# Kernel tuning notes

Hardware: AMD Instinct MI355X
Metric: run time of the kernel (lower is better)

The kernel has to match this reference:

```python
import jax, jax.numpy as jnp
import numpy as np

B, T, C, H = 16, 2048, 768, 128

def setup_inputs() -> dict:
    key = jax.random.key(0)
    k1, k2, k3, k4 = jax.random.split(key, 4)
    x = jax.random.normal(k1, (B, T, C), dtype=jnp.float32)
    Wq = jax.random.normal(k2, (C, H), dtype=jnp.float32) * (C ** -0.5)
    Wk = jax.random.normal(k3, (C, H), dtype=jnp.float32) * (C ** -0.5)
    Wv = jax.random.normal(k4, (C, H), dtype=jnp.float32) * (C ** -0.5)
    return {"x": x, "Wq": Wq, "Wk": Wk, "Wv": Wv}

def reference(x, Wq, Wk, Wv):
    Bc, Tc, Cc = x.shape
    q = jnp.einsum('btc,ch->bth', x, Wq)
    k = jnp.einsum('btc,ch->bth', x, Wk)
    v = jnp.einsum('btc,ch->bth', x, Wv)
    wei = jnp.einsum('bqh,bkh->bqk', q, k)  # [B,T,T]
    tril = jnp.tril(jnp.ones((Tc, Tc), dtype=jnp.float32))
    # Faithful to original: mask with -inf FIRST, then scale by C**-0.5
    wei = jnp.where(tril == 0, -jnp.inf, wei) * (Cc ** -0.5)
    wei = jax.nn.softmax(wei, axis=-1)
    out = jnp.einsum('bqk,bkh->bqh', wei, v)
    return out
```

## Files before the change

### kernel.cpp

```cpp
#include <hip/hip_runtime.h>
#include <hip/hip_bf16.h>
#include <cstdint>

#define B_ 16
#define T_ 2048
#define C_ 768
#define H_ 128

typedef __bf16 bf16x8 __attribute__((ext_vector_type(8)));
typedef float f32x4 __attribute__((ext_vector_type(4)));
typedef unsigned short u16x8 __attribute__((ext_vector_type(8)));

__device__ __forceinline__ void gld_lds16(const void* g, void* s) {
    __builtin_amdgcn_global_load_lds(
        (__attribute__((address_space(1))) void*)(size_t)g,
        (__attribute__((address_space(3))) void*)s,
        16, 0, 0);
}

__device__ __forceinline__ unsigned short f2bf(float f) {
    __bf16 h = (__bf16)f;
    return __builtin_bit_cast(unsigned short, h);
}

__global__ __launch_bounds__(256) void wxconv_kernel(
    const float* __restrict__ Wq, const float* __restrict__ Wk,
    const float* __restrict__ Wv, const float* __restrict__ x,
    unsigned short* __restrict__ wT, unsigned short* __restrict__ xb) {
    int bidx = blockIdx.x;
    if (bidx < 1152) {
        int idx = bidx * 256 + threadIdx.x;
        if (idx >= 3 * H_ * C_) return;
        int w = idx / (H_ * C_);
        int r = idx % (H_ * C_);
        int h = r / C_;
        int c = r % C_;
        const float* W = (w == 0) ? Wq : ((w == 1) ? Wk : Wv);
        wT[idx] = f2bf(W[c * H_ + h]);
    } else {
        size_t i = ((size_t)(bidx - 1152) * 256 + threadIdx.x) * 8;
        f32x4 a = *(const f32x4*)(x + i);
        f32x4 b = *(const f32x4*)(x + i + 4);
        u16x8 o;
        o[0] = f2bf(a[0]); o[1] = f2bf(a[1]); o[2] = f2bf(a[2]); o[3] = f2bf(a[3]);
        o[4] = f2bf(b[0]); o[5] = f2bf(b[1]); o[6] = f2bf(b[2]); o[7] = f2bf(b[3]);
        *(u16x8*)(xb + i) = o;
    }
}

__global__ __launch_bounds__(256, 2) void proj_kernel(
    const unsigned short* __restrict__ xb, const unsigned short* __restrict__ wT,
    unsigned short* __restrict__ qb, unsigned short* __restrict__ kb,
    unsigned short* __restrict__ vtb) {
    __shared__ unsigned short Asm[64 * 64];
    __shared__ unsigned short Bsm[384 * 64];

    const int tid = threadIdx.x;
    const int m0 = blockIdx.x * 64;
    const int wid = tid >> 6;
    const int lane = tid & 63;
    const int quad = lane >> 4;
    const int lo16 = lane & 15;
    const int wn = wid * 96;

    f32x4 acc[4][6] = {};

    for (int kt = 0; kt < 12; ++kt) {
        const int k0 = kt * 64;
        __syncthreads();
#pragma unroll
        for (int rnd = 0; rnd < 2; ++rnd) {
            int cidx = rnd * 256 + tid;
            int m = cidx >> 3;
            int c = (cidx & 7) ^ (m & 7);
            gld_lds16((const char*)xb + ((size_t)(m0 + m) * C_ + k0 + c * 8) * 2,
                      (char*)Asm + (rnd * 256 + wid * 64) * 16);
        }
#pragma unroll
        for (int rnd = 0; rnd < 12; ++rnd) {
            int cidx = rnd * 256 + tid;
            int n = cidx >> 3;
            int c = (cidx & 7) ^ (n & 7);
            gld_lds16((const char*)wT + ((size_t)(n >> 7) * (H_ * C_) + (n & 127) * C_ + k0 + c * 8) * 2,
                      (char*)Bsm + (rnd * 256 + wid * 64) * 16);
        }
        __syncthreads();

#pragma unroll
        for (int kk = 0; kk < 2; ++kk) {
            bf16x8 afrag[4], bfrag[6];
#pragma unroll
            for (int mi = 0; mi < 4; ++mi) {
                int m = mi * 16 + lo16;
                int c = (kk * 4 + quad) ^ (m & 7);
                afrag[mi] = *(const bf16x8*)((const __bf16*)Asm + m * 64 + c * 8);
            }
#pragma unroll
            for (int ni = 0; ni < 6; ++ni) {
                int n = wn + ni * 16 + lo16;
                int c = (kk * 4 + quad) ^ (n & 7);
                bfrag[ni] = *(const bf16x8*)((const __bf16*)Bsm + n * 64 + c * 8);
            }
#pragma unroll
            for (int mi = 0; mi < 4; ++mi)
#pragma unroll
                for (int ni = 0; ni < 6; ++ni)
                    acc[mi][ni] = __builtin_amdgcn_mfma_f32_16x16x32_bf16(
                        afrag[mi], bfrag[ni], acc[mi][ni], 0, 0, 0);
        }
    }

#pragma unroll
    for (int mi = 0; mi < 4; ++mi) {
        int grow = m0 + mi * 16 + quad * 4;
#pragma unroll
        for (int ni = 0; ni < 6; ++ni) {
            int n = wn + ni * 16 + lo16;
            int wmat = n >> 7;
            int col = n & 127;
            if (wmat < 2) {
                unsigned short* o = (wmat == 0) ? qb : kb;
#pragma unroll
                for (int rr = 0; rr < 4; ++rr)
                    o[(size_t)(grow + rr) * H_ + col] = f2bf(acc[mi][ni][rr]);
            } else {
                int b = grow >> 11;
                int t = grow & 2047;
                ushort4 pk;
                pk.x = f2bf(acc[mi][ni][0]); pk.y = f2bf(acc[mi][ni][1]);
                pk.z = f2bf(acc[mi][ni][2]); pk.w = f2bf(acc[mi][ni][3]);
                *(ushort4*)(vtb + ((size_t)b * H_ + col) * T_ + t) = pk;
            }
        }
    }
}

__device__ __forceinline__ void attn_seg(
    const unsigned short* kB, const unsigned short* vB, const bf16x8 qfrag[4],
    int j0, int j1, int jmask, float& l_part, f32x4 oacc[8],
    unsigned short* Ks, unsigned short* Vs, unsigned short* Pw,
    int tid, int wid, int quad, int lo16) {
    const float cs = 0.05205877694341f;
    for (int j = j0; j < j1; ++j) {
        const int kv0 = j * 64;
        __syncthreads();
#pragma unroll
        for (int rnd = 0; rnd < 4; ++rnd) {
            int cidx = rnd * 256 + tid;
            int m = cidx >> 4;
            int c = (cidx & 15) ^ (m & 15);
            gld_lds16((const char*)kB + ((size_t)(kv0 + m) * H_ + c * 8) * 2,
                      (char*)Ks + (rnd * 256 + wid * 64) * 16);
        }
#pragma unroll
        for (int rnd = 0; rnd < 4; ++rnd) {
            int cidx = rnd * 256 + tid;
            int d = cidx >> 3;
            int c = (cidx & 7) ^ (d & 7);
            gld_lds16((const char*)vB + ((size_t)d * T_ + kv0 + c * 8) * 2,
                      (char*)Vs + (rnd * 256 + wid * 64) * 16);
        }
        __syncthreads();

        f32x4 s[4] = {};
#pragma unroll
        for (int ks = 0; ks < 4; ++ks) {
#pragma unroll
            for (int ni = 0; ni < 4; ++ni) {
                int row = ni * 16 + lo16;
                int slot = (ks * 4 + quad) ^ lo16;
                bf16x8 kf = *(const bf16x8*)((const __bf16*)Ks + row * 128 + slot * 8);
                s[ni] = __builtin_amdgcn_mfma_f32_16x16x32_bf16(kf, qfrag[ks], s[ni], 0, 0, 0);
            }
        }

        const bool diag = (j == jmask);
        if (diag) {
#pragma unroll
            for (int ni = 0; ni < 4; ++ni) {
#pragma unroll
                for (int rr = 0; rr < 4; ++rr) {
                    float p = exp2f(s[ni][rr] * cs);
                    if (ni * 16 + quad * 4 + rr > wid * 16 + lo16) p = 0.f;
                    l_part += p;
                    s[ni][rr] = p;
                }
                ushort4 w4;
                w4.x = f2bf(s[ni][0]); w4.y = f2bf(s[ni][1]);
                w4.z = f2bf(s[ni][2]); w4.w = f2bf(s[ni][3]);
                *(ushort4*)(Pw + lo16 * 72 + ni * 16 + quad * 4) = w4;
            }
        } else {
#pragma unroll
            for (int ni = 0; ni < 4; ++ni) {
#pragma unroll
                for (int rr = 0; rr < 4; ++rr) {
                    float p = exp2f(s[ni][rr] * cs);
                    l_part += p;
                    s[ni][rr] = p;
                }
                ushort4 w4;
                w4.x = f2bf(s[ni][0]); w4.y = f2bf(s[ni][1]);
                w4.z = f2bf(s[ni][2]); w4.w = f2bf(s[ni][3]);
                *(ushort4*)(Pw + lo16 * 72 + ni * 16 + quad * 4) = w4;
            }
        }

#pragma unroll
        for (int ks2 = 0; ks2 < 2; ++ks2) {
            bf16x8 pf = *(const bf16x8*)((const __bf16*)Pw + lo16 * 72 + ks2 * 32 + quad * 8);
#pragma unroll
            for (int nd = 0; nd < 8; ++nd) {
                int dn = nd * 16 + lo16;
                int vc = (ks2 * 4 + quad) ^ (dn & 7);
                bf16x8 vf = *(const bf16x8*)((const __bf16*)Vs + dn * 64 + vc * 8);
                oacc[nd] = __builtin_amdgcn_mfma_f32_16x16x32_bf16(pf, vf, oacc[nd], 0, 0, 0);
            }
        }
    }
}

__device__ __forceinline__ void load_qfrag(const unsigned short* qB, int q0,
                                           int wid, int quad, int lo16, bf16x8 qf[4]) {
    const unsigned short* qrow = qB + (size_t)(q0 + wid * 16 + lo16) * H_ + quad * 8;
#pragma unroll
    for (int ks = 0; ks < 4; ++ks) qf[ks] = *(const bf16x8*)(qrow + ks * 32);
}

__global__ __launch_bounds__(256, 2) void attn_kernel(
    const unsigned short* __restrict__ qb, const unsigned short* __restrict__ kb,
    const unsigned short* __restrict__ vtb, float* __restrict__ out,
    float* __restrict__ pO, float* __restrict__ pL) {
    __shared__ unsigned short Ks[64 * 128];
    __shared__ unsigned short Vs[128 * 64];
    __shared__ unsigned short Ps[4][16 * 72];

    const int tid = threadIdx.x;
    const int bid = blockIdx.x;
    const int half = bid >> 8;
    const int slot = bid & 255;
    const int r = slot >> 4;
    const int b = slot & 15;

    const unsigned short* qB = qb + (size_t)b * T_ * H_;
    const unsigned short* kB = kb + (size_t)b * T_ * H_;
    const unsigned short* vB = vtb + (size_t)b * H_ * T_;

    const int wid = tid >> 6;
    const int lane = tid & 63;
    const int quad = lane >> 4;
    const int lo16 = lane & 15;
    unsigned short* Pw = &Ps[wid][0];

    const int qtb = 31 - r;
    bf16x8 qf[4];
    float l_part = 0.f;
    f32x4 oacc[8] = {};

    if (half == 0) {
        load_qfrag(qB, r * 64, wid, quad, lo16, qf);
        attn_seg(kB, vB, qf, 0, r + 1, r, l_part, oacc, Ks, Vs, Pw, tid, wid, quad, lo16);
        l_part += __shfl_xor(l_part, 16);
        l_part += __shfl_xor(l_part, 32);
#pragma unroll
        for (int rr = 0; rr < 4; ++rr) {
            float lv = __shfl(l_part, quad * 4 + rr);
            float inv = 1.0f / lv;
            int qrow = r * 64 + wid * 16 + quad * 4 + rr;
            float* orow = out + ((size_t)b * T_ + qrow) * H_;
#pragma unroll
            for (int nd = 0; nd < 8; ++nd)
                orow[nd * 16 + lo16] = oacc[nd][rr] * inv;
        }
        l_part = 0.f;
#pragma unroll
        for (int nd = 0; nd < 8; ++nd) oacc[nd] = f32x4{0.f, 0.f, 0.f, 0.f};
        load_qfrag(qB, qtb * 64, wid, quad, lo16, qf);
        attn_seg(kB, vB, qf, 0, 16 - r, -1, l_part, oacc, Ks, Vs, Pw, tid, wid, quad, lo16);
    } else {
        load_qfrag(qB, qtb * 64, wid, quad, lo16, qf);
        attn_seg(kB, vB, qf, 16 - r, 32 - r, qtb, l_part, oacc, Ks, Vs, Pw, tid, wid, quad, lo16);
    }

    l_part += __shfl_xor(l_part, 16);
    l_part += __shfl_xor(l_part, 32);
    float* myO = pO + (size_t)(half * 256 + slot) * (64 * 128);
    if (lane < 16) pL[(half * 256 + slot) * 64 + wid * 16 + lo16] = l_part;
#pragma unroll
    for (int rr = 0; rr < 4; ++rr) {
        int ql = wid * 16 + quad * 4 + rr;
#pragma unroll
        for (int nd = 0; nd < 8; ++nd)
            myO[ql * 128 + nd * 16 + lo16] = oacc[nd][rr];
    }
}

__global__ __launch_bounds__(256) void combine_kernel(
    const float* __restrict__ pO, const float* __restrict__ pL,
    float* __restrict__ out) {
    const int slot = blockIdx.x;
    const int r = slot >> 4;
    const int b = slot & 15;
    const int q0 = (31 - r) * 64;
    __shared__ float ls[64];
    const int tid = threadIdx.x;
    if (tid < 64) ls[tid] = pL[slot * 64 + tid] + pL[(256 + slot) * 64 + tid];
    __syncthreads();
    const float* O0 = pO + (size_t)slot * (64 * 128);
    const float* O1 = pO + (size_t)(256 + slot) * (64 * 128);
    float* ob = out + ((size_t)b * T_ + q0) * H_;
#pragma unroll
    for (int k = 0; k < 8; ++k) {
        int idx = (k * 256 + tid) * 4;
        f32x4 a = *(const f32x4*)(O0 + idx);
        f32x4 c = *(const f32x4*)(O1 + idx);
        float inv = 1.0f / ls[idx >> 7];
        f32x4 o;
        o[0] = (a[0] + c[0]) * inv; o[1] = (a[1] + c[1]) * inv;
        o[2] = (a[2] + c[2]) * inv; o[3] = (a[3] + c[3]) * inv;
        *(f32x4*)(ob + idx) = o;
    }
}

extern "C" void kernel_launch(void* const* d_in, const int* in_sizes, int n_in,
                              void* d_out, int out_size, void* d_ws, size_t ws_size,
                              hipStream_t stream) {
    const float* x = (const float*)d_in[0];
    const float* Wq = (const float*)d_in[1];
    const float* Wk = (const float*)d_in[2];
    const float* Wv = (const float*)d_in[3];
    float* out = (float*)d_out;

    char* ws = (char*)d_ws;
    unsigned short* wT  = (unsigned short*)ws;
    unsigned short* qb  = (unsigned short*)(ws + (1ull << 20));
    unsigned short* kb  = (unsigned short*)(ws + (9ull << 20));
    unsigned short* vtb = (unsigned short*)(ws + (17ull << 20));
    unsigned short* xb  = (unsigned short*)(ws + (25ull << 20));
    float* pO = (float*)(ws + (80ull << 20));
    float* pL = (float*)(ws + (100ull << 20));

    hipLaunchKernelGGL(wxconv_kernel, dim3(13440), dim3(256), 0, stream, Wq, Wk, Wv, x, wT, xb);
    hipLaunchKernelGGL(proj_kernel, dim3(512), dim3(256), 0, stream, xb, wT, qb, kb, vtb);
    hipLaunchKernelGGL(attn_kernel, dim3(512), dim3(256), 0, stream, qb, kb, vtb, out, pO, pL);
    hipLaunchKernelGGL(combine_kernel, dim3(256), dim3(256), 0, stream, pO, pL, out);
}
```

Baseline: 221.6 us.

## Fuse x bf16 conversion into projection and double-buffer projection and attention tiles

The separate x-to-bf16 conversion pass is removed. The projection kernel now reads fp32 x directly, converts it in registers and writes it into LDS. Projection is retiled into 512-thread blocks of 128 rows by 192 columns, with double-buffered LDS so the next k-slice loads while MFMAs run. Attention also double-buffers its K/V tiles, issuing the next tile's async loads before computing on the current one, which drops one barrier per iteration. This costs more LDS, which may reduce occupancy, and adds register pressure from the fp32 prefetch.

```diff
diff --git a/kernel.cpp b/kernel.cpp
--- a/kernel.cpp
+++ b/kernel.cpp
@@ -23,99 +23,136 @@
     return __builtin_bit_cast(unsigned short, h);
 }
 
-__global__ __launch_bounds__(256) void wxconv_kernel(
+__global__ __launch_bounds__(256) void wconv_kernel(
     const float* __restrict__ Wq, const float* __restrict__ Wk,
-    const float* __restrict__ Wv, const float* __restrict__ x,
-    unsigned short* __restrict__ wT, unsigned short* __restrict__ xb) {
-    int bidx = blockIdx.x;
-    if (bidx < 1152) {
-        int idx = bidx * 256 + threadIdx.x;
-        if (idx >= 3 * H_ * C_) return;
-        int w = idx / (H_ * C_);
-        int r = idx % (H_ * C_);
-        int h = r / C_;
-        int c = r % C_;
-        const float* W = (w == 0) ? Wq : ((w == 1) ? Wk : Wv);
-        wT[idx] = f2bf(W[c * H_ + h]);
-    } else {
-        size_t i = ((size_t)(bidx - 1152) * 256 + threadIdx.x) * 8;
-        f32x4 a = *(const f32x4*)(x + i);
-        f32x4 b = *(const f32x4*)(x + i + 4);
-        u16x8 o;
-        o[0] = f2bf(a[0]); o[1] = f2bf(a[1]); o[2] = f2bf(a[2]); o[3] = f2bf(a[3]);
-        o[4] = f2bf(b[0]); o[5] = f2bf(b[1]); o[6] = f2bf(b[2]); o[7] = f2bf(b[3]);
-        *(u16x8*)(xb + i) = o;
-    }
-}
-
-__global__ __launch_bounds__(256, 2) void proj_kernel(
-    const unsigned short* __restrict__ xb, const unsigned short* __restrict__ wT,
+    const float* __restrict__ Wv, unsigned short* __restrict__ wT) {
+    int idx = blockIdx.x * 256 + threadIdx.x;
+    if (idx >= 3 * H_ * C_) return;
+    int w = idx / (H_ * C_);
+    int r = idx % (H_ * C_);
+    int h = r / C_;
+    int c = r % C_;
+    const float* W = (w == 0) ? Wq : ((w == 1) ? Wk : Wv);
+    wT[idx] = f2bf(W[c * H_ + h]);
+}
+
+__global__ __launch_bounds__(512, 2) void proj_kernel(
+    const float* __restrict__ x, const unsigned short* __restrict__ wT,
     unsigned short* __restrict__ qb, unsigned short* __restrict__ kb,
     unsigned short* __restrict__ vtb) {
-    __shared__ unsigned short Asm[64 * 64];
-    __shared__ unsigned short Bsm[384 * 64];
+    __shared__ unsigned short Asm[2][128 * 64];
+    __shared__ unsigned short Bsm[2][192 * 64];
 
     const int tid = threadIdx.x;
-    const int m0 = blockIdx.x * 64;
+    const int nh = blockIdx.x & 1;
+    const int m0 = (blockIdx.x >> 1) * 128;
     const int wid = tid >> 6;
     const int lane = tid & 63;
     const int quad = lane >> 4;
     const int lo16 = lane & 15;
-    const int wn = wid * 96;
-
-    f32x4 acc[4][6] = {};
+    const int mh = (wid >> 2) * 64;
+    const int wnl = (wid & 3) * 48;
+    const unsigned short* wTn = wT + (size_t)nh * 192 * C_;
+
+    const int am0 = (tid * 2) >> 4;
+    (void)am0;
+
+    f32x4 acc[4][3] = {};
+    f32x4 pre[4];
+
+#pragma unroll
+    for (int r = 0; r < 2; ++r) {
+        int cidx = r * 512 + tid;
+        int m = cidx >> 3, lc = cidx & 7;
+        const float* src = x + (size_t)(m0 + m) * C_ + lc * 8;
+        pre[r * 2] = *(const f32x4*)src;
+        pre[r * 2 + 1] = *(const f32x4*)(src + 4);
+    }
+#pragma unroll
+    for (int r = 0; r < 3; ++r) {
+        int cidx = r * 512 + tid;
+        int n = cidx >> 3, c = (cidx & 7) ^ (n & 7);
+        gld_lds16((const char*)wTn + ((size_t)n * C_ + c * 8) * 2,
+                  (char*)&Bsm[0][0] + (r * 512 + wid * 64) * 16);
+    }
+#pragma unroll
+    for (int r = 0; r < 2; ++r) {
+        int cidx = r * 512 + tid;
+        int m = cidx >> 3, lc = cidx & 7;
+        u16x8 o;
+        o[0] = f2bf(pre[r * 2][0]); o[1] = f2bf(pre[r * 2][1]);
+        o[2] = f2bf(pre[r * 2][2]); o[3] = f2bf(pre[r * 2][3]);
+        o[4] = f2bf(pre[r * 2 + 1][0]); o[5] = f2bf(pre[r * 2 + 1][1]);
+        o[6] = f2bf(pre[r * 2 + 1][2]); o[7] = f2bf(pre[r * 2 + 1][3]);
+        *(u16x8*)(&Asm[0][m * 64 + (lc ^ (m & 7)) * 8]) = o;
+    }
 
     for (int kt = 0; kt < 12; ++kt) {
-        const int k0 = kt * 64;
+        const int p = kt & 1;
         __syncthreads();
-#pragma unroll
-        for (int rnd = 0; rnd < 2; ++rnd) {
-            int cidx = rnd * 256 + tid;
-            int m = cidx >> 3;
-            int c = (cidx & 7) ^ (m & 7);
-            gld_lds16((const char*)xb + ((size_t)(m0 + m) * C_ + k0 + c * 8) * 2,
-                      (char*)Asm + (rnd * 256 + wid * 64) * 16);
-        }
-#pragma unroll
-        for (int rnd = 0; rnd < 12; ++rnd) {
-            int cidx = rnd * 256 + tid;
-            int n = cidx >> 3;
-            int c = (cidx & 7) ^ (n & 7);
-            gld_lds16((const char*)wT + ((size_t)(n >> 7) * (H_ * C_) + (n & 127) * C_ + k0 + c * 8) * 2,
-                      (char*)Bsm + (rnd * 256 + wid * 64) * 16);
-        }
-        __syncthreads();
+        if (kt + 1 < 12) {
+            const int k1 = (kt + 1) * 64;
+#pragma unroll
+            for (int r = 0; r < 2; ++r) {
+                int cidx = r * 512 + tid;
+                int m = cidx >> 3, lc = cidx & 7;
+                const float* src = x + (size_t)(m0 + m) * C_ + k1 + lc * 8;
+                pre[r * 2] = *(const f32x4*)src;
+                pre[r * 2 + 1] = *(const f32x4*)(src + 4);
+            }
+#pragma unroll
+            for (int r = 0; r < 3; ++r) {
+                int cidx = r * 512 + tid;
+                int n = cidx >> 3, c = (cidx & 7) ^ (n & 7);
+                gld_lds16((const char*)wTn + ((size_t)n * C_ + k1 + c * 8) * 2,
+                          (char*)&Bsm[p ^ 1][0] + (r * 512 + wid * 64) * 16);
+            }
+        }
 
 #pragma unroll
         for (int kk = 0; kk < 2; ++kk) {
-            bf16x8 afrag[4], bfrag[6];
+            bf16x8 af[4], bf[3];
 #pragma unroll
             for (int mi = 0; mi < 4; ++mi) {
-                int m = mi * 16 + lo16;
+                int m = mh + mi * 16 + lo16;
                 int c = (kk * 4 + quad) ^ (m & 7);
-                afrag[mi] = *(const bf16x8*)((const __bf16*)Asm + m * 64 + c * 8);
-            }
-#pragma unroll
-            for (int ni = 0; ni < 6; ++ni) {
-                int n = wn + ni * 16 + lo16;
+                af[mi] = *(const bf16x8*)((const __bf16*)&Asm[p][0] + m * 64 + c * 8);
+            }
+#pragma unroll
+            for (int ni = 0; ni < 3; ++ni) {
+                int n = wnl + ni * 16 + lo16;
                 int c = (kk * 4 + quad) ^ (n & 7);
-                bfrag[ni] = *(const bf16x8*)((const __bf16*)Bsm + n * 64 + c * 8);
+                bf[ni] = *(const bf16x8*)((const __bf16*)&Bsm[p][0] + n * 64 + c * 8);
             }
 #pragma unroll
             for (int mi = 0; mi < 4; ++mi)
 #pragma unroll
-                for (int ni = 0; ni < 6; ++ni)
+                for (int ni = 0; ni < 3; ++ni)
                     acc[mi][ni] = __builtin_amdgcn_mfma_f32_16x16x32_bf16(
-                        afrag[mi], bfrag[ni], acc[mi][ni], 0, 0, 0);
+                        af[mi], bf[ni], acc[mi][ni], 0, 0, 0);
+        }
+
+        if (kt + 1 < 12) {
+#pragma unroll
+            for (int r = 0; r < 2; ++r) {
+                int cidx = r * 512 + tid;
+                int m = cidx >> 3, lc = cidx & 7;
+                u16x8 o;
+                o[0] = f2bf(pre[r * 2][0]); o[1] = f2bf(pre[r * 2][1]);
+                o[2] = f2bf(pre[r * 2][2]); o[3] = f2bf(pre[r * 2][3]);
+                o[4] = f2bf(pre[r * 2 + 1][0]); o[5] = f2bf(pre[r * 2 + 1][1]);
+                o[6] = f2bf(pre[r * 2 + 1][2]); o[7] = f2bf(pre[r * 2 + 1][3]);
+                *(u16x8*)(&Asm[p ^ 1][m * 64 + (lc ^ (m & 7)) * 8]) = o;
+            }
         }
     }
 
 #pragma unroll
     for (int mi = 0; mi < 4; ++mi) {
-        int grow = m0 + mi * 16 + quad * 4;
-#pragma unroll
-        for (int ni = 0; ni < 6; ++ni) {
-            int n = wn + ni * 16 + lo16;
+        int grow = m0 + mh + mi * 16 + quad * 4;
+#pragma unroll
+        for (int ni = 0; ni < 3; ++ni) {
+            int n = nh * 192 + wnl + ni * 16 + lo16;
             int wmat = n >> 7;
             int col = n & 127;
             if (wmat < 2) {
@@ -135,32 +172,42 @@
     }
 }
 
+__device__ __forceinline__ void attn_stage(
+    const unsigned short* kB, const unsigned short* vB, int kv0, int p,
+    unsigned short* Ks, unsigned short* Vs, int tid, int wid) {
+#pragma unroll
+    for (int rnd = 0; rnd < 4; ++rnd) {
+        int cidx = rnd * 256 + tid;
+        int m = cidx >> 4;
+        int c = (cidx & 15) ^ (m & 15);
+        gld_lds16((const char*)kB + ((size_t)(kv0 + m) * H_ + c * 8) * 2,
+                  (char*)(Ks + p * 64 * 128) + (rnd * 256 + wid * 64) * 16);
+    }
+#pragma unroll
+    for (int rnd = 0; rnd < 4; ++rnd) {
+        int cidx = rnd * 256 + tid;
+        int d = cidx >> 3;
+        int c = (cidx & 7) ^ (d & 7);
+        gld_lds16((const char*)vB + ((size_t)d * T_ + kv0 + c * 8) * 2,
+                  (char*)(Vs + p * 128 * 64) + (rnd * 256 + wid * 64) * 16);
+    }
+}
+
 __device__ __forceinline__ void attn_seg(
     const unsigned short* kB, const unsigned short* vB, const bf16x8 qfrag[4],
     int j0, int j1, int jmask, float& l_part, f32x4 oacc[8],
     unsigned short* Ks, unsigned short* Vs, unsigned short* Pw,
     int tid, int wid, int quad, int lo16) {
     const float cs = 0.05205877694341f;
+    __syncthreads();
+    attn_stage(kB, vB, j0 * 64, 0, Ks, Vs, tid, wid);
     for (int j = j0; j < j1; ++j) {
-        const int kv0 = j * 64;
+        const int p = (j - j0) & 1;
         __syncthreads();
-#pragma unroll
-        for (int rnd = 0; rnd < 4; ++rnd) {
-            int cidx = rnd * 256 + tid;
-            int m = cidx >> 4;
-            int c = (cidx & 15) ^ (m & 15);
-            gld_lds16((const char*)kB + ((size_t)(kv0 + m) * H_ + c * 8) * 2,
-                      (char*)Ks + (rnd * 256 + wid * 64) * 16);
-        }
-#pragma unroll
-        for (int rnd = 0; rnd < 4; ++rnd) {
-            int cidx = rnd * 256 + tid;
-            int d = cidx >> 3;
-            int c = (cidx & 7) ^ (d & 7);
-            gld_lds16((const char*)vB + ((size_t)d * T_ + kv0 + c * 8) * 2,
-                      (char*)Vs + (rnd * 256 + wid * 64) * 16);
-        }
-        __syncthreads();
+        if (j + 1 < j1) attn_stage(kB, vB, (j + 1) * 64, p ^ 1, Ks, Vs, tid, wid);
+
+        const unsigned short* Kp = Ks + p * 64 * 128;
+        const unsigned short* Vp = Vs + p * 128 * 64;
 
         f32x4 s[4] = {};
 #pragma unroll
@@ -169,7 +216,7 @@
             for (int ni = 0; ni < 4; ++ni) {
                 int row = ni * 16 + lo16;
                 int slot = (ks * 4 + quad) ^ lo16;
-                bf16x8 kf = *(const bf16x8*)((const __bf16*)Ks + row * 128 + slot * 8);
+                bf16x8 kf = *(const bf16x8*)((const __bf16*)Kp + row * 128 + slot * 8);
                 s[ni] = __builtin_amdgcn_mfma_f32_16x16x32_bf16(kf, qfrag[ks], s[ni], 0, 0, 0);
             }
         }
@@ -180,10 +227,10 @@
             for (int ni = 0; ni < 4; ++ni) {
 #pragma unroll
                 for (int rr = 0; rr < 4; ++rr) {
-                    float p = exp2f(s[ni][rr] * cs);
-                    if (ni * 16 + quad * 4 + rr > wid * 16 + lo16) p = 0.f;
-                    l_part += p;
-                    s[ni][rr] = p;
+                    float pv = exp2f(s[ni][rr] * cs);
+                    if (ni * 16 + quad * 4 + rr > wid * 16 + lo16) pv = 0.f;
+                    l_part += pv;
+                    s[ni][rr] = pv;
                 }
                 ushort4 w4;
                 w4.x = f2bf(s[ni][0]); w4.y = f2bf(s[ni][1]);
@@ -195,9 +242,9 @@
             for (int ni = 0; ni < 4; ++ni) {
 #pragma unroll
                 for (int rr = 0; rr < 4; ++rr) {
-                    float p = exp2f(s[ni][rr] * cs);
-                    l_part += p;
-                    s[ni][rr] = p;
+                    float pv = exp2f(s[ni][rr] * cs);
+                    l_part += pv;
+                    s[ni][rr] = pv;
                 }
                 ushort4 w4;
                 w4.x = f2bf(s[ni][0]); w4.y = f2bf(s[ni][1]);
@@ -213,7 +260,7 @@
             for (int nd = 0; nd < 8; ++nd) {
                 int dn = nd * 16 + lo16;
                 int vc = (ks2 * 4 + quad) ^ (dn & 7);
-                bf16x8 vf = *(const bf16x8*)((const __bf16*)Vs + dn * 64 + vc * 8);
+                bf16x8 vf = *(const bf16x8*)((const __bf16*)Vp + dn * 64 + vc * 8);
                 oacc[nd] = __builtin_amdgcn_mfma_f32_16x16x32_bf16(pf, vf, oacc[nd], 0, 0, 0);
             }
         }
@@ -231,8 +278,8 @@
     const unsigned short* __restrict__ qb, const unsigned short* __restrict__ kb,
     const unsigned short* __restrict__ vtb, float* __restrict__ out,
     float* __restrict__ pO, float* __restrict__ pL) {
-    __shared__ unsigned short Ks[64 * 128];
-    __shared__ unsigned short Vs[128 * 64];
+    __shared__ unsigned short Ks[2][64 * 128];
+    __shared__ unsigned short Vs[2][128 * 64];
     __shared__ unsigned short Ps[4][16 * 72];
 
     const int tid = threadIdx.x;
@@ -259,7 +306,8 @@
 
     if (half == 0) {
         load_qfrag(qB, r * 64, wid, quad, lo16, qf);
-        attn_seg(kB, vB, qf, 0, r + 1, r, l_part, oacc, Ks, Vs, Pw, tid, wid, quad, lo16);
+        attn_seg(kB, vB, qf, 0, r + 1, r, l_part, oacc, &Ks[0][0], &Vs[0][0], Pw,
+                 tid, wid, quad, lo16);
         l_part += __shfl_xor(l_part, 16);
         l_part += __shfl_xor(l_part, 32);
 #pragma unroll
@@ -276,10 +324,12 @@
 #pragma unroll
         for (int nd = 0; nd < 8; ++nd) oacc[nd] = f32x4{0.f, 0.f, 0.f, 0.f};
         load_qfrag(qB, qtb * 64, wid, quad, lo16, qf);
-        attn_seg(kB, vB, qf, 0, 16 - r, -1, l_part, oacc, Ks, Vs, Pw, tid, wid, quad, lo16);
+        attn_seg(kB, vB, qf, 0, 16 - r, -1, l_part, oacc, &Ks[0][0], &Vs[0][0], Pw,
+                 tid, wid, quad, lo16);
     } else {
         load_qfrag(qB, qtb * 64, wid, quad, lo16, qf);
-        attn_seg(kB, vB, qf, 16 - r, 32 - r, qtb, l_part, oacc, Ks, Vs, Pw, tid, wid, quad, lo16);
+        attn_seg(kB, vB, qf, 16 - r, 32 - r, qtb, l_part, oacc, &Ks[0][0], &Vs[0][0], Pw,
+                 tid, wid, quad, lo16);
     }
 
     l_part += __shfl_xor(l_part, 16);
@@ -336,12 +386,11 @@
     unsigned short* qb  = (unsigned short*)(ws + (1ull << 20));
     unsigned short* kb  = (unsigned short*)(ws + (9ull << 20));
     unsigned short* vtb = (unsigned short*)(ws + (17ull << 20));
-    unsigned short* xb  = (unsigned short*)(ws + (25ull << 20));
     float* pO = (float*)(ws + (80ull << 20));
     float* pL = (float*)(ws + (100ull << 20));
 
-    hipLaunchKernelGGL(wxconv_kernel, dim3(13440), dim3(256), 0, stream, Wq, Wk, Wv, x, wT, xb);
-    hipLaunchKernelGGL(proj_kernel, dim3(512), dim3(256), 0, stream, xb, wT, qb, kb, vtb);
+    hipLaunchKernelGGL(wconv_kernel, dim3(1152), dim3(256), 0, stream, Wq, Wk, Wv, wT);
+    hipLaunchKernelGGL(proj_kernel, dim3(512), dim3(512), 0, stream, x, wT, qb, kb, vtb);
     hipLaunchKernelGGL(attn_kernel, dim3(512), dim3(256), 0, stream, qb, kb, vtb, out, pO, pL);
     hipLaunchKernelGGL(combine_kernel, dim3(256), dim3(256), 0, stream, pO, pL, out);
 }
```

Measured after the change: 211.6 us. 1.05x faster.
